# Optimization experiments

Measured on AMD Instinct MI355X. Metric: run time of the kernel, lower is better.

## Reference

```python
import jax, jax.numpy as jnp
import numpy as np

B, S, H = 2, 2048, 2048
NH, NKV = 16, 4
HD = H // NH            # 128
GROUPS = NH // NKV      # 4
ROTARY_BASE = 10000.0
NEG = -1e9


def setup_inputs() -> dict:
    key = jax.random.key(0)
    ks = jax.random.split(key, 6)
    x = jax.random.normal(ks[0], (B, S, H), dtype=jnp.float32)
    # additive causal mask [B,1,S,S]
    causal = jnp.where(jnp.tril(jnp.ones((S, S), dtype=bool)), 0.0, NEG).astype(jnp.float32)
    attention_mask = jnp.broadcast_to(causal[None, None], (B, 1, S, S))
    position_ids = jnp.broadcast_to(jnp.arange(S, dtype=jnp.int32)[None], (B, S))
    sc = 0.02
    Wq = jax.random.normal(ks[1], (H, NH * HD), dtype=jnp.float32) * sc
    Wk = jax.random.normal(ks[2], (H, NKV * HD), dtype=jnp.float32) * sc
    Wv = jax.random.normal(ks[3], (H, NKV * HD), dtype=jnp.float32) * sc
    Wo = jax.random.normal(ks[4], (H, H), dtype=jnp.float32) * sc
    return {"x": x, "attention_mask": attention_mask, "position_ids": position_ids,
            "Wq": Wq, "Wk": Wk, "Wv": Wv, "Wo": Wo}


def _rotate_half(t):
    t1, t2 = t[..., : HD // 2], t[..., HD // 2:]
    return jnp.concatenate((-t2, t1), axis=-1)


def _rope_sin_cos(position_ids, dtype):
    inv_freq = 1.0 / (ROTARY_BASE ** (jnp.arange(0, HD, 2, dtype=jnp.float32) / HD))  # [HD/2]
    freqs = position_ids.astype(jnp.float32)[..., None] * inv_freq[None, None, :]      # [B,S,HD/2]
    emb = jnp.concatenate((freqs, freqs), axis=-1)                                     # [B,S,HD]
    return jnp.sin(emb).astype(dtype), jnp.cos(emb).astype(dtype)


def reference(x, attention_mask, position_ids, Wq, Wk, Wv, Wo):
    # QKV projections (no bias)
    q = (x @ Wq).reshape(B, S, NH, HD).transpose(0, 2, 1, 3)     # [B,NH,S,HD]
    k = (x @ Wk).reshape(B, S, NKV, HD).transpose(0, 2, 1, 3)    # [B,NKV,S,HD]
    v = (x @ Wv).reshape(B, S, NKV, HD).transpose(0, 2, 1, 3)
    sin, cos = _rope_sin_cos(position_ids, x.dtype)
    sin, cos = sin[:, None], cos[:, None]                         # unsqueeze head dim
    q = q * cos + _rotate_half(q) * sin
    k = k * cos + _rotate_half(k) * sin
    # GQA: repeat kv heads
    k = jnp.repeat(k, GROUPS, axis=1)                             # [B,NH,S,HD]
    v = jnp.repeat(v, GROUPS, axis=1)
    scores = jnp.einsum('bhqd,bhkd->bhqk', q, k) / jnp.sqrt(jnp.asarray(HD, x.dtype))
    scores = scores + attention_mask                              # additive causal mask
    attn = jax.nn.softmax(scores.astype(jnp.float32), axis=-1).astype(x.dtype)
    # dropout p=0.0 -> no-op
    out = jnp.einsum('bhqk,bhkd->bhqd', attn, v)                  # [B,NH,S,HD]
    out = out.transpose(0, 2, 1, 3).reshape(B, S, H)
    return out @ Wo
```

## Files before the change

### kernel.cpp

```cpp
#include <hip/hip_runtime.h>
#include <hip/hip_bf16.h>
#include <stdint.h>
#include <math.h>

#define B_ 2
#define S_ 2048
#define H_ 2048
#define NH_ 16
#define NKV_ 4
#define HD_ 128

typedef __bf16 bf16;
typedef __bf16 bf16x8 __attribute__((ext_vector_type(8)));
typedef __bf16 bf16x4 __attribute__((ext_vector_type(4)));
typedef float f32x4 __attribute__((ext_vector_type(4)));

__device__ __forceinline__ void async_copy16(const void* g, void* l) {
  __builtin_amdgcn_global_load_lds(
      (const __attribute__((address_space(1))) void*)(uintptr_t)g,
      (__attribute__((address_space(3))) void*)(uintptr_t)l,
      16, 0, 0);
}

__device__ __forceinline__ f32x4 mfma16(bf16x8 a, bf16x8 b, f32x4 c) {
  return __builtin_amdgcn_mfma_f32_16x16x32_bf16(a, b, c, 0, 0, 0);
}


__global__ void f32_to_bf16_k(const float* __restrict__ in, bf16* __restrict__ o, int n) {
  int i = (blockIdx.x * 256 + threadIdx.x) * 4;
  if (i >= n) return;
  float4 v = *(const float4*)(in + i);
  bf16x4 r;
  r[0] = (bf16)v.x; r[1] = (bf16)v.y; r[2] = (bf16)v.z; r[3] = (bf16)v.w;
  *(bf16x4*)(o + i) = r;
}

__global__ void transpose_all_k(const float* __restrict__ Wq, const float* __restrict__ Wk,
                                const float* __restrict__ Wv, const float* __restrict__ Wo,
                                bf16* __restrict__ WqkvT, bf16* __restrict__ WoT) {
  __shared__ float tile[32][33];
  int bid = blockIdx.x;
  const float* W; bf16* Wt; int N, bx, by;
  if (bid < 4096)      { W = Wq; Wt = WqkvT;                          N = 2048; int b2 = bid;        bx = b2 & 63; by = b2 >> 6; }
  else if (bid < 5120) { W = Wk; Wt = WqkvT + (size_t)2048 * 2048;    N = 512;  int b2 = bid - 4096; bx = b2 & 15; by = b2 >> 4; }
  else if (bid < 6144) { W = Wv; Wt = WqkvT + (size_t)2560 * 2048;    N = 512;  int b2 = bid - 5120; bx = b2 & 15; by = b2 >> 4; }
  else                 { W = Wo; Wt = WoT;                            N = 2048; int b2 = bid - 6144; bx = b2 & 63; by = b2 >> 6; }
  const int K = 2048;
  int n0 = bx * 32, k0 = by * 32;
  int tx = threadIdx.x, ty = threadIdx.y;
#pragma unroll
  for (int j = 0; j < 32; j += 8)
    tile[ty + j][tx] = W[(size_t)(k0 + ty + j) * N + n0 + tx];
  __syncthreads();
#pragma unroll
  for (int j = 0; j < 32; j += 8)
    Wt[(size_t)(n0 + ty + j) * K + k0 + tx] = (bf16)tile[tx][ty + j];
}

__global__ void rope_table_k(float2* __restrict__ tab) {
  int i = blockIdx.x * 256 + threadIdx.x;
  int p = i >> 6, d = i & 63;
  float invf = expf(-((float)(2 * d) / 128.0f) * 9.210340371976184f);
  float fr = (float)p * invf;
  float sv, cv;
  sincosf(fr, &sv, &cv);
  tab[i] = make_float2(cv, sv);
}

__global__ void rope_apply_v8_k(bf16* __restrict__ t, const int* __restrict__ pos_ids,
                                const float2* __restrict__ tab, int hshift, int hmask,
                                float scale) {
  int i = blockIdx.x * 256 + threadIdx.x;
  int g = i & 7;
  int tmp = i >> 3;
  int h = tmp & hmask;
  int row = tmp >> hshift;
  int pos = pos_ids[row];
  size_t base = (((size_t)row << hshift) + h) * HD_ + g * 8;
  const float2* tb = tab + pos * 64 + g * 8;
  bf16x8 lo = *(const bf16x8*)(t + base);
  bf16x8 hi = *(const bf16x8*)(t + base + 64);
  float4 t0 = *(const float4*)(tb);
  float4 t1 = *(const float4*)(tb + 2);
  float4 t2 = *(const float4*)(tb + 4);
  float4 t3 = *(const float4*)(tb + 6);
  float cs[8], sn[8];
  cs[0]=t0.x; sn[0]=t0.y; cs[1]=t0.z; sn[1]=t0.w;
  cs[2]=t1.x; sn[2]=t1.y; cs[3]=t1.z; sn[3]=t1.w;
  cs[4]=t2.x; sn[4]=t2.y; cs[5]=t2.z; sn[5]=t2.w;
  cs[6]=t3.x; sn[6]=t3.y; cs[7]=t3.z; sn[7]=t3.w;
  bf16x8 olo, ohi;
#pragma unroll
  for (int j = 0; j < 8; ++j) {
    float a = (float)lo[j], b = (float)hi[j];
    olo[j] = (bf16)((a * cs[j] - b * sn[j]) * scale);
    ohi[j] = (bf16)((b * cs[j] + a * sn[j]) * scale);
  }
  *(bf16x8*)(t + base) = olo;
  *(bf16x8*)(t + base + 64) = ohi;
}


template <int MODE, int NJ>
__global__ __launch_bounds__(512) void gemm256_k(const bf16* __restrict__ A,
                                                 const bf16* __restrict__ Bt,
                                                 void* __restrict__ C0,
                                                 void* __restrict__ C1,
                                                 void* __restrict__ C2,
                                                 int M, int N, int K) {
  extern __shared__ __align__(16) char smem[];
  constexpr int BUFSZ = 32768 + NJ * 8192;
  const int tid = threadIdx.x;
  const int lane = tid & 63;
  const int w = tid >> 6;
  const int wm = w >> 2;
  const int wn = w & 3;
  const int g16 = lane >> 4, c16 = lane & 15;
  const int row0 = blockIdx.y * 256;
  const int col0 = blockIdx.x * (NJ * 64);
  const int srow = tid >> 3;
  const int sslot = tid & 7;
  const int ldsw = w * 1024;

  auto stage = [&](int buf, int kt, int r) {
    int rr = (r < 4) ? r : r - 4;
    int row = rr * 64 + srow;
    int ss = sslot ^ (row & 7);
    const bf16* src = (r < 4) ? (A + (size_t)(row0 + row) * K)
                              : (Bt + (size_t)(col0 + row) * K);
    async_copy16(src + (kt << 6) + ss * 8,
                 smem + buf * BUFSZ + ((r < 4) ? 0 : 32768) + rr * 8192 + ldsw);
  };

  int offA[2][8], offB[2][NJ];
#pragma unroll
  for (int ks = 0; ks < 2; ++ks) {
#pragma unroll
    for (int i = 0; i < 8; ++i) {
      int ra = wm * 128 + i * 16 + c16;
      offA[ks][i] = ra * 128 + (((ks * 4 + g16) ^ (ra & 7)) << 4);
    }
#pragma unroll
    for (int j = 0; j < NJ; ++j) {
      int rb = wn * (16 * NJ) + j * 16 + c16;
      offB[ks][j] = 32768 + rb * 128 + (((ks * 4 + g16) ^ (rb & 7)) << 4);
    }
  }

  const f32x4 fz = {0.f, 0.f, 0.f, 0.f};
  f32x4 acc[8][NJ];
#pragma unroll
  for (int i = 0; i < 8; ++i)
#pragma unroll
    for (int j = 0; j < NJ; ++j) acc[i][j] = fz;

  const int nkt = K >> 6;
#pragma unroll
  for (int r = 0; r < 4 + NJ; ++r) stage(0, 0, r);
  asm volatile("s_waitcnt vmcnt(0)" ::: "memory");
  __builtin_amdgcn_s_barrier();

  for (int t = 0; t < nkt; ++t) {
    const char* Ab = smem + (t & 1) * BUFSZ;
    const bool pf = (t + 1 < nkt);
    const int nb = (t + 1) & 1;
    bf16x8 bfr[2][NJ];

    {
      bf16x8 af[2][2];
#pragma unroll
      for (int ks = 0; ks < 2; ++ks) {
#pragma unroll
        for (int j = 0; j < NJ; ++j) bfr[ks][j] = *(const bf16x8*)(Ab + offB[ks][j]);
        af[ks][0] = *(const bf16x8*)(Ab + offA[ks][0]);
        af[ks][1] = *(const bf16x8*)(Ab + offA[ks][1]);
      }
      if (pf) { stage(nb, t + 1, 0); stage(nb, t + 1, 1); stage(nb, t + 1, 2); stage(nb, t + 1, 3); }
      __builtin_amdgcn_s_barrier();
      asm volatile("s_waitcnt lgkmcnt(0)" ::: "memory");
      __builtin_amdgcn_sched_barrier(0);
      __builtin_amdgcn_s_setprio(1);
#pragma unroll
      for (int ks = 0; ks < 2; ++ks)
#pragma unroll
        for (int m = 0; m < 2; ++m)
#pragma unroll
          for (int j = 0; j < NJ; ++j)
            acc[m][j] = mfma16(af[ks][m], bfr[ks][j], acc[m][j]);
      __builtin_amdgcn_s_setprio(0);
      __builtin_amdgcn_sched_barrier(0);
      __builtin_amdgcn_s_barrier();
    }

#pragma unroll
    for (int q = 1; q < 4; ++q) {
      bf16x8 af[2][2];
#pragma unroll
      for (int ks = 0; ks < 2; ++ks) {
        af[ks][0] = *(const bf16x8*)(Ab + offA[ks][q * 2]);
        af[ks][1] = *(const bf16x8*)(Ab + offA[ks][q * 2 + 1]);
      }
      if (q == 1 && pf) {
#pragma unroll
        for (int r = 0; r < NJ; ++r) stage(nb, t + 1, 4 + r);
      }
      __builtin_amdgcn_s_barrier();
      asm volatile("s_waitcnt lgkmcnt(0)" ::: "memory");
      __builtin_amdgcn_sched_barrier(0);
      __builtin_amdgcn_s_setprio(1);
#pragma unroll
      for (int ks = 0; ks < 2; ++ks)
#pragma unroll
        for (int m = 0; m < 2; ++m)
#pragma unroll
          for (int j = 0; j < NJ; ++j)
            acc[q * 2 + m][j] = mfma16(af[ks][m], bfr[ks][j], acc[q * 2 + m][j]);
      __builtin_amdgcn_s_setprio(0);
      __builtin_amdgcn_sched_barrier(0);
      if (q == 3 && pf) asm volatile("s_waitcnt vmcnt(0)" ::: "memory");
      __builtin_amdgcn_s_barrier();
    }
  }

#pragma unroll
  for (int i = 0; i < 8; ++i) {
    int gr0 = row0 + wm * 128 + i * 16 + g16 * 4;
#pragma unroll
    for (int j = 0; j < NJ; ++j) {
      int gc = col0 + wn * (16 * NJ) + j * 16 + c16;
      if constexpr (MODE == 2) {
        if (gc < 2048) {
#pragma unroll
          for (int r = 0; r < 4; ++r)
            ((bf16*)C0)[(size_t)(gr0 + r) * 2048 + gc] = (bf16)acc[i][j][r];
        } else if (gc < 2560) {
#pragma unroll
          for (int r = 0; r < 4; ++r)
            ((bf16*)C1)[(size_t)(gr0 + r) * 512 + (gc - 2048)] = (bf16)acc[i][j][r];
        } else {
          int dv = gc - 2560;
          int hkv = dv >> 7, d = dv & 127;
          size_t va = (((size_t)(gr0 >> 11) * NKV_ + hkv) * HD_ + d) * S_ + (gr0 & 2047);
          bf16x4 pk;
#pragma unroll
          for (int r = 0; r < 4; ++r) pk[r] = (bf16)acc[i][j][r];
          *(bf16x4*)((bf16*)C2 + va) = pk;
        }
      } else {
#pragma unroll
        for (int r = 0; r < 4; ++r) {
          if constexpr (MODE == 1)
            ((float*)C0)[(size_t)(gr0 + r) * N + gc] = acc[i][j][r];
          else
            ((bf16*)C0)[(size_t)(gr0 + r) * N + gc] = (bf16)acc[i][j][r];
        }
      }
    }
  }
}


template <int MODE>
__global__ __launch_bounds__(512) void gemm8_k(const bf16* __restrict__ A,
                                               const bf16* __restrict__ Bt,
                                               void* __restrict__ C0,
                                               void* __restrict__ C1,
                                               void* __restrict__ C2,
                                               int M, int N, int K) {
  extern __shared__ __align__(16) char smem[];
  const int tid = threadIdx.x;
  const int lane = tid & 63;
  const int w = tid >> 6;
  const int wm = w >> 2;
  const int wn = w & 3;
  const int g16 = lane >> 4, c16 = lane & 15;
  const int row0 = blockIdx.y * 128;
  const int col0 = blockIdx.x * 256;
  const int srow = tid >> 3;
  const int sslot = tid & 7;
  const int ldsw = w * 1024;

  auto stageA = [&](int s, int kt, int r) {
    int row = r * 64 + srow;
    int ss = sslot ^ (row & 7);
    async_copy16(A + (size_t)(row0 + row) * K + (kt << 6) + ss * 8,
                 smem + s * 49152 + r * 8192 + ldsw);
  };
  auto stageB = [&](int s, int kt, int r) {
    int row = r * 64 + srow;
    int ss = sslot ^ (row & 7);
    async_copy16(Bt + (size_t)(col0 + row) * K + (kt << 6) + ss * 8,
                 smem + s * 49152 + 16384 + r * 8192 + ldsw);
  };

  int offA[2][4], offB[2][4];
#pragma unroll
  for (int ks = 0; ks < 2; ++ks) {
#pragma unroll
    for (int i = 0; i < 4; ++i) {
      int ra = wm * 64 + i * 16 + c16;
      offA[ks][i] = ra * 128 + (((ks * 4 + g16) ^ (ra & 7)) << 4);
      int rb = wn * 64 + i * 16 + c16;
      offB[ks][i] = rb * 128 + (((ks * 4 + g16) ^ (rb & 7)) << 4);
    }
  }

  const f32x4 fz = {0.f, 0.f, 0.f, 0.f};
  f32x4 acc[4][4];
#pragma unroll
  for (int i = 0; i < 4; ++i)
#pragma unroll
    for (int j = 0; j < 4; ++j) acc[i][j] = fz;

  const int nkt = K >> 6;
#pragma unroll
  for (int r = 0; r < 2; ++r) stageA(0, 0, r);
#pragma unroll
  for (int r = 0; r < 4; ++r) stageB(0, 0, r);
#pragma unroll
  for (int r = 0; r < 2; ++r) stageA(1, 1, r);
#pragma unroll
  for (int r = 0; r < 4; ++r) stageB(1, 1, r);
  asm volatile("s_waitcnt vmcnt(6)" ::: "memory");
  __builtin_amdgcn_s_barrier();

  int ct = 0, pt = 2;
  for (int t = 0; t < nkt; ++t) {
    const char* Ab = smem + ct * 49152;
    const char* Bb = Ab + 16384;
    const bool pf = (t + 2 < nkt);
    const int kpf = t + 2;
    bf16x8 af[4], bfr[4];

#pragma unroll
    for (int i = 0; i < 4; ++i) af[i] = *(const bf16x8*)(Ab + offA[0][i]);
#pragma unroll
    for (int j = 0; j < 4; ++j) bfr[j] = *(const bf16x8*)(Bb + offB[0][j]);
    if (pf) { stageA(pt, kpf, 0); stageA(pt, kpf, 1); stageB(pt, kpf, 0); }
    __builtin_amdgcn_s_barrier();
    asm volatile("s_waitcnt lgkmcnt(0)" ::: "memory");
    __builtin_amdgcn_sched_barrier(0);
    __builtin_amdgcn_s_setprio(1);
#pragma unroll
    for (int i = 0; i < 4; ++i)
#pragma unroll
      for (int j = 0; j < 4; ++j) acc[i][j] = mfma16(af[i], bfr[j], acc[i][j]);
    __builtin_amdgcn_s_setprio(0);
    __builtin_amdgcn_sched_barrier(0);
    __builtin_amdgcn_s_barrier();

#pragma unroll
    for (int i = 0; i < 4; ++i) af[i] = *(const bf16x8*)(Ab + offA[1][i]);
#pragma unroll
    for (int j = 0; j < 4; ++j) bfr[j] = *(const bf16x8*)(Bb + offB[1][j]);
    if (pf) { stageB(pt, kpf, 1); stageB(pt, kpf, 2); stageB(pt, kpf, 3); }
    if (pf) asm volatile("s_waitcnt vmcnt(6)" ::: "memory");
    else    asm volatile("s_waitcnt vmcnt(0)" ::: "memory");
    __builtin_amdgcn_s_barrier();
    asm volatile("s_waitcnt lgkmcnt(0)" ::: "memory");
    __builtin_amdgcn_sched_barrier(0);
    __builtin_amdgcn_s_setprio(1);
#pragma unroll
    for (int i = 0; i < 4; ++i)
#pragma unroll
      for (int j = 0; j < 4; ++j) acc[i][j] = mfma16(af[i], bfr[j], acc[i][j]);
    __builtin_amdgcn_s_setprio(0);
    __builtin_amdgcn_sched_barrier(0);
    __builtin_amdgcn_s_barrier();

    ct = (ct == 2) ? 0 : ct + 1;
    pt = (pt == 2) ? 0 : pt + 1;
  }

#pragma unroll
  for (int i = 0; i < 4; ++i) {
    int gr0 = row0 + wm * 64 + i * 16 + g16 * 4;
#pragma unroll
    for (int j = 0; j < 4; ++j) {
      int gc = col0 + wn * 64 + j * 16 + c16;
#pragma unroll
      for (int r = 0; r < 4; ++r) {
        if constexpr (MODE == 1)
          ((float*)C0)[(size_t)(gr0 + r) * N + gc] = acc[i][j][r];
        else
          ((bf16*)C0)[(size_t)(gr0 + r) * N + gc] = (bf16)acc[i][j][r];
      }
    }
  }
}


__global__ __launch_bounds__(256, 2) void attn_fwd_k(const bf16* __restrict__ Qg,
                                                     const bf16* __restrict__ Kg,
                                                     const bf16* __restrict__ VTg,
                                                     bf16* __restrict__ Og) {
  __shared__ __align__(16) bf16 Ks[2][64 * 128];
  __shared__ __align__(16) bf16 Vt[3][128 * 64];

  const int tid = threadIdx.x;
  const int lane = tid & 63;
  const int w = tid >> 6;
  const int g16 = lane >> 4;
  const int c16 = lane & 15;

  int bid = blockIdx.x;
  int rr_ = bid >> 5, bh = bid & 31;
  int qb = (rr_ < 8) ? (15 - rr_) : (rr_ - 8);
  const int b = bh >> 4;
  const int h = bh & 15;
  const int hkv = h >> 2;
  const int q0 = qb * 128;
  const int qw = q0 + w * 32;

  bf16x8 qf[2][4];
#pragma unroll
  for (int nq = 0; nq < 2; ++nq)
#pragma unroll
    for (int ksq = 0; ksq < 4; ++ksq)
      qf[nq][ksq] = *(const bf16x8*)(Qg + ((size_t)(b * S_ + qw + nq * 16 + c16) * NH_ + h) * HD_ + (ksq * 4 + g16) * 8);

  float m_run[2] = {-1e30f, -1e30f};
  float l_run[2] = {0.f, 0.f};
  const f32x4 fz = {0.f, 0.f, 0.f, 0.f};
  f32x4 acc[2][8];
#pragma unroll
  for (int nq = 0; nq < 2; ++nq)
#pragma unroll
    for (int dt = 0; dt < 8; ++dt) acc[nq][dt] = fz;

  const size_t kbase = ((size_t)b * S_ * NKV_ + hkv) * HD_;
  const size_t vbase = ((size_t)(b * NKV_ + hkv)) * HD_ * S_;

  auto stageK = [&](int buf, int kv0) {
#pragma unroll
    for (int rd = 0; rd < 4; ++rd) {
      int Lb = rd * 256 + w * 64;
      int row = (Lb + lane) >> 4;
      int ssl = (lane & 15) ^ (row & 7);
      async_copy16(Kg + kbase + (size_t)(kv0 + row) * (NKV_ * HD_) + ssl * 8,
                   (char*)&Ks[buf][0] + Lb * 16);
    }
  };
  auto stageV = [&](int buf, int kv0) {
#pragma unroll
    for (int rd = 0; rd < 4; ++rd) {
      int Lb = rd * 256 + w * 64;
      int row = (Lb + lane) >> 3;
      int ssl = (lane & 7) ^ (row & 7);
      async_copy16(VTg + vbase + (size_t)row * S_ + kv0 + ssl * 8,
                   (char*)&Vt[buf][0] + Lb * 16);
    }
  };

  const int ntiles = 2 * qb + 2;
  stageK(0, 0);
  stageV(0, 0);

  bf16x8 pa[2][2];
  bool pend = false;
  int vb_pend = 0;
  int vbt = 0;

  for (int t = 0; t < ntiles; ++t) {
    __syncthreads();
    int vbn = (vbt == 2) ? 0 : vbt + 1;
    if (t + 1 < ntiles) { stageK((t + 1) & 1, (t + 1) * 64); stageV(vbn, (t + 1) * 64); }
    const int kv0 = t * 64;
    const bool g = (kv0 <= qw + 31);

    f32x4 sc[2][4];
    if (g) {
      const char* KsC = (const char*)&Ks[t & 1][0];
#pragma unroll
      for (int nq = 0; nq < 2; ++nq)
#pragma unroll
        for (int mt = 0; mt < 4; ++mt) sc[nq][mt] = fz;

      __builtin_amdgcn_s_setprio(1);
#pragma unroll
      for (int ksq = 0; ksq < 4; ++ksq) {
        bf16x8 kf[4];
#pragma unroll
        for (int mt = 0; mt < 4; ++mt) {
          int gp = c16 >> 2, rp = c16 & 3;
          int blk = 8 * (mt >> 1) + 2 * gp + ((mt & 1) ^ (gp & 1));
          int row = blk * 4 + rp;
          kf[mt] = *(const bf16x8*)(KsC + row * 256 + (((ksq * 4 + g16) ^ (row & 7)) << 4));
        }
#pragma unroll
        for (int nq = 0; nq < 2; ++nq)
#pragma unroll
          for (int mt = 0; mt < 4; ++mt)
            sc[nq][mt] = mfma16(kf[mt], qf[nq][ksq], sc[nq][mt]);
      }
      __builtin_amdgcn_s_setprio(0);
    }

    if (pend) {
      const char* VtP = (const char*)&Vt[vb_pend][0];
      __builtin_amdgcn_s_setprio(1);
#pragma unroll
      for (int ks = 0; ks < 2; ++ks)
#pragma unroll
        for (int dt = 0; dt < 8; ++dt) {
          int rv = dt * 16 + c16;
          bf16x8 vf = *(const bf16x8*)(VtP + rv * 128 + (((ks * 4 + g16) ^ (rv & 7)) << 4));
          acc[0][dt] = mfma16(vf, pa[0][ks], acc[0][dt]);
          acc[1][dt] = mfma16(vf, pa[1][ks], acc[1][dt]);
        }
      __builtin_amdgcn_s_setprio(0);
      pend = false;
    }

    if (g) {
      if (kv0 + 63 > qw) {
#pragma unroll
        for (int nq = 0; nq < 2; ++nq) {
          int qa = qw + nq * 16 + c16;
#pragma unroll
          for (int mt = 0; mt < 4; ++mt) {
            int blk = 8 * (mt >> 1) + 2 * g16 + ((mt & 1) ^ (g16 & 1));
#pragma unroll
            for (int r = 0; r < 4; ++r) {
              int ka = kv0 + blk * 4 + r;
              if (ka > qa) sc[nq][mt][r] = -1e30f;
            }
          }
        }
      }

      float mx[2];
#pragma unroll
      for (int nq = 0; nq < 2; ++nq) {
        float v = sc[nq][0][0];
#pragma unroll
        for (int mt = 0; mt < 4; ++mt)
#pragma unroll
          for (int r = 0; r < 4; ++r) v = fmaxf(v, sc[nq][mt][r]);
        v = fmaxf(v, __shfl_xor(v, 16));
        v = fmaxf(v, __shfl_xor(v, 32));
        mx[nq] = v;
      }
      if (__any((mx[0] > m_run[0] + 8.f) || (mx[1] > m_run[1] + 8.f))) {
#pragma unroll
        for (int nq = 0; nq < 2; ++nq) {
          float mn = fmaxf(m_run[nq], mx[nq]);
          float corr = exp2f(m_run[nq] - mn);
          m_run[nq] = mn;
          l_run[nq] *= corr;
#pragma unroll
          for (int dt = 0; dt < 8; ++dt) acc[nq][dt] *= corr;
        }
      }
#pragma unroll
      for (int nq = 0; nq < 2; ++nq) {
        float sum = 0.f;
#pragma unroll
        for (int mt = 0; mt < 4; ++mt)
#pragma unroll
          for (int r = 0; r < 4; ++r) {
            float p = exp2f(sc[nq][mt][r] - m_run[nq]);
            sc[nq][mt][r] = p;
            sum += p;
          }
        sum += __shfl_xor(sum, 16);
        sum += __shfl_xor(sum, 32);
        l_run[nq] += sum;
      }

#pragma unroll
      for (int nq = 0; nq < 2; ++nq)
#pragma unroll
        for (int ks = 0; ks < 2; ++ks) {
          f32x4 sA = (g16 & 1) ? sc[nq][2 * ks + 1] : sc[nq][2 * ks];
          f32x4 sB = (g16 & 1) ? sc[nq][2 * ks] : sc[nq][2 * ks + 1];
          bf16x8 tf;
          tf[0] = (bf16)sA[0]; tf[1] = (bf16)sA[1]; tf[2] = (bf16)sA[2]; tf[3] = (bf16)sA[3];
          tf[4] = (bf16)sB[0]; tf[5] = (bf16)sB[1]; tf[6] = (bf16)sB[2]; tf[7] = (bf16)sB[3];
          pa[nq][ks] = tf;
        }
      pend = true;
      vb_pend = vbt;
    }
    vbt = vbn;
  }

  if (pend) {
    const char* VtP = (const char*)&Vt[vb_pend][0];
#pragma unroll
    for (int ks = 0; ks < 2; ++ks)
#pragma unroll
      for (int dt = 0; dt < 8; ++dt) {
        int rv = dt * 16 + c16;
        bf16x8 vf = *(const bf16x8*)(VtP + rv * 128 + (((ks * 4 + g16) ^ (rv & 7)) << 4));
        acc[0][dt] = mfma16(vf, pa[0][ks], acc[0][dt]);
        acc[1][dt] = mfma16(vf, pa[1][ks], acc[1][dt]);
      }
  }

#pragma unroll
  for (int nq = 0; nq < 2; ++nq) {
    float inv = 1.0f / l_run[nq];
    size_t base = ((size_t)(b * S_ + qw + nq * 16 + c16) * NH_ + h) * HD_ + g16 * 4;
#pragma unroll
    for (int dt = 0; dt < 8; ++dt) {
      bf16x4 ov;
#pragma unroll
      for (int r = 0; r < 4; ++r) ov[r] = (bf16)(acc[nq][dt][r] * inv);
      *(bf16x4*)(Og + base + dt * 16) = ov;
    }
  }
}


extern "C" void kernel_launch(void* const* d_in, const int* in_sizes, int n_in,
                              void* d_out, int out_size, void* d_ws, size_t ws_size,
                              hipStream_t stream) {
  const float* x  = (const float*)d_in[0];
  const int* pos  = (const int*)d_in[2];
  const float* Wq = (const float*)d_in[3];
  const float* Wk = (const float*)d_in[4];
  const float* Wv = (const float*)d_in[5];
  const float* Wo = (const float*)d_in[6];

  char* ws = (char*)d_ws;
  size_t off = 0;
  auto alloc = [&](size_t bytes) -> char* {
    char* p = ws + off;
    off += (bytes + 255) & ~(size_t)255;
    return p;
  };
  const size_t rows = (size_t)B_ * S_;
  bf16* xb    = (bf16*)alloc(rows * H_ * 2);
  bf16* bq    = (bf16*)alloc(rows * (NH_ * HD_) * 2);
  bf16* batt  = (bf16*)alloc(rows * (NH_ * HD_) * 2);
  bf16* WqkvT = (bf16*)alloc((size_t)3072 * H_ * 2);
  bf16* WoT   = (bf16*)alloc((size_t)H_ * H_ * 2);
  bf16* bk    = (bf16*)alloc(rows * (NKV_ * HD_) * 2);
  bf16* VT    = (bf16*)alloc(rows * (NKV_ * HD_) * 2);
  float2* tab = (float2*)alloc((size_t)S_ * 64 * sizeof(float2));

  auto* fqkv = gemm256_k<2, 3>;
  auto* fo   = gemm8_k<1>;
  const int lds256 = 2 * (32768 + 3 * 8192);
  const int lds8   = 3 * 49152;
  bool big =
      (hipFuncSetAttribute((const void*)fqkv, hipFuncAttributeMaxDynamicSharedMemorySize, lds256) == hipSuccess) &&
      (hipFuncSetAttribute((const void*)fo, hipFuncAttributeMaxDynamicSharedMemorySize, lds8) == hipSuccess);

  f32_to_bf16_k<<<(rows * H_) / (256 * 4), 256, 0, stream>>>(x, xb, rows * H_);
  transpose_all_k<<<10240, dim3(32, 8), 0, stream>>>(Wq, Wk, Wv, Wo, WqkvT, WoT);
  rope_table_k<<<(S_ * 64) / 256, 256, 0, stream>>>(tab);

  gemm256_k<2, 3><<<dim3(16, 16), 512, lds256, stream>>>(xb, WqkvT, bq, bk, VT, 4096, 3072, 2048);
  (void)big;

  rope_apply_v8_k<<<(4096 * NH_ * 8) / 256, 256, 0, stream>>>(bq, pos, tab, 4, 15, 0.12753102f);
  rope_apply_v8_k<<<(4096 * NKV_ * 8) / 256, 256, 0, stream>>>(bk, pos, tab, 2, 3, 1.0f);

  attn_fwd_k<<<dim3(512), 256, 0, stream>>>(bq, bk, VT, batt);

  gemm8_k<1><<<dim3(8, 32), 512, lds8, stream>>>(batt, WoT, d_out, nullptr, nullptr, 4096, 2048, 2048);
}
```

Baseline: 199.2 us.

## Merge prep kernels, simplify attention pipeline, reorder causal block scheduling

Merges the fp32-to-bf16 cast, weight transposes and RoPE table build into one launch to cut launch overhead. Replaces the attention kernel's deferred PV software pipeline (triple-buffered V) with a simpler double buffer where PV runs right after softmax in the same iteration. Also remaps block indices so heavy and light causal q-blocks are interleaved across the grid. The PV step no longer overlaps the next tile's QK and softmax work, which may expose latency, but the kernel uses less LDS and fewer registers.

```diff
diff --git a/kernel.cpp b/kernel.cpp
--- a/kernel.cpp
+++ b/kernel.cpp
@@ -27,45 +27,46 @@
 }
 
 
-__global__ void f32_to_bf16_k(const float* __restrict__ in, bf16* __restrict__ o, int n) {
-  int i = (blockIdx.x * 256 + threadIdx.x) * 4;
-  if (i >= n) return;
-  float4 v = *(const float4*)(in + i);
-  bf16x4 r;
-  r[0] = (bf16)v.x; r[1] = (bf16)v.y; r[2] = (bf16)v.z; r[3] = (bf16)v.w;
-  *(bf16x4*)(o + i) = r;
-}
-
-__global__ void transpose_all_k(const float* __restrict__ Wq, const float* __restrict__ Wk,
-                                const float* __restrict__ Wv, const float* __restrict__ Wo,
-                                bf16* __restrict__ WqkvT, bf16* __restrict__ WoT) {
+__global__ void prep_all_k(const float* __restrict__ x,
+                           const float* __restrict__ Wq, const float* __restrict__ Wk,
+                           const float* __restrict__ Wv, const float* __restrict__ Wo,
+                           bf16* __restrict__ xb, bf16* __restrict__ WqkvT,
+                           bf16* __restrict__ WoT, float2* __restrict__ tab) {
   __shared__ float tile[32][33];
-  int bid = blockIdx.x;
-  const float* W; bf16* Wt; int N, bx, by;
-  if (bid < 4096)      { W = Wq; Wt = WqkvT;                          N = 2048; int b2 = bid;        bx = b2 & 63; by = b2 >> 6; }
-  else if (bid < 5120) { W = Wk; Wt = WqkvT + (size_t)2048 * 2048;    N = 512;  int b2 = bid - 4096; bx = b2 & 15; by = b2 >> 4; }
-  else if (bid < 6144) { W = Wv; Wt = WqkvT + (size_t)2560 * 2048;    N = 512;  int b2 = bid - 5120; bx = b2 & 15; by = b2 >> 4; }
-  else                 { W = Wo; Wt = WoT;                            N = 2048; int b2 = bid - 6144; bx = b2 & 63; by = b2 >> 6; }
-  const int K = 2048;
-  int n0 = bx * 32, k0 = by * 32;
-  int tx = threadIdx.x, ty = threadIdx.y;
-#pragma unroll
-  for (int j = 0; j < 32; j += 8)
-    tile[ty + j][tx] = W[(size_t)(k0 + ty + j) * N + n0 + tx];
-  __syncthreads();
-#pragma unroll
-  for (int j = 0; j < 32; j += 8)
-    Wt[(size_t)(n0 + ty + j) * K + k0 + tx] = (bf16)tile[tx][ty + j];
-}
-
-__global__ void rope_table_k(float2* __restrict__ tab) {
-  int i = blockIdx.x * 256 + threadIdx.x;
-  int p = i >> 6, d = i & 63;
-  float invf = expf(-((float)(2 * d) / 128.0f) * 9.210340371976184f);
-  float fr = (float)p * invf;
-  float sv, cv;
-  sincosf(fr, &sv, &cv);
-  tab[i] = make_float2(cv, sv);
+  const int bid = blockIdx.x;
+  const int tid = threadIdx.x;
+
+  if (bid < 10240) {
+    const float* W; bf16* Wt; int N, bx, by;
+    if (bid < 4096)      { W = Wq; Wt = WqkvT;                       N = 2048; int b2 = bid;        bx = b2 & 63; by = b2 >> 6; }
+    else if (bid < 5120) { W = Wk; Wt = WqkvT + (size_t)2048 * 2048; N = 512;  int b2 = bid - 4096; bx = b2 & 15; by = b2 >> 4; }
+    else if (bid < 6144) { W = Wv; Wt = WqkvT + (size_t)2560 * 2048; N = 512;  int b2 = bid - 5120; bx = b2 & 15; by = b2 >> 4; }
+    else                 { W = Wo; Wt = WoT;                         N = 2048; int b2 = bid - 6144; bx = b2 & 63; by = b2 >> 6; }
+    const int K = 2048;
+    int n0 = bx * 32, k0 = by * 32;
+    int tx = tid & 31, ty = tid >> 5;
+#pragma unroll
+    for (int j = 0; j < 32; j += 8)
+      tile[ty + j][tx] = W[(size_t)(k0 + ty + j) * N + n0 + tx];
+    __syncthreads();
+#pragma unroll
+    for (int j = 0; j < 32; j += 8)
+      Wt[(size_t)(n0 + ty + j) * K + k0 + tx] = (bf16)tile[tx][ty + j];
+  } else if (bid < 18432) {
+    int i = ((bid - 10240) * 256 + tid) * 4;
+    float4 v = *(const float4*)(x + i);
+    bf16x4 r;
+    r[0] = (bf16)v.x; r[1] = (bf16)v.y; r[2] = (bf16)v.z; r[3] = (bf16)v.w;
+    *(bf16x4*)(xb + i) = r;
+  } else {
+    int i = (bid - 18432) * 256 + tid;
+    int p = i >> 6, d = i & 63;
+    float invf = expf(-((float)(2 * d) / 128.0f) * 9.210340371976184f);
+    float fr = (float)p * invf;
+    float sv, cv;
+    sincosf(fr, &sv, &cv);
+    tab[i] = make_float2(cv, sv);
+  }
 }
 
 __global__ void rope_apply_v8_k(bf16* __restrict__ t, const int* __restrict__ pos_ids,
@@ -396,7 +397,7 @@
                                                      const bf16* __restrict__ VTg,
                                                      bf16* __restrict__ Og) {
   __shared__ __align__(16) bf16 Ks[2][64 * 128];
-  __shared__ __align__(16) bf16 Vt[3][128 * 64];
+  __shared__ __align__(16) bf16 Vt[2][128 * 64];
 
   const int tid = threadIdx.x;
   const int lane = tid & 63;
@@ -404,9 +405,11 @@
   const int g16 = lane >> 4;
   const int c16 = lane & 15;
 
-  int bid = blockIdx.x;
-  int rr_ = bid >> 5, bh = bid & 31;
-  int qb = (rr_ < 8) ? (15 - rr_) : (rr_ - 8);
+  const int bid = blockIdx.x;
+  const int i_ = ((bid >> 8) << 7) | ((bid & 255) >> 1);
+  const int par = ((bid & 1) ^ (bid >> 8)) & 1;
+  const int qb = par ? (i_ >> 5) : (15 - (i_ >> 5));
+  const int bh = i_ & 31;
   const int b = bh >> 4;
   const int h = bh & 15;
   const int hkv = h >> 2;
@@ -432,7 +435,7 @@
   const size_t kbase = ((size_t)b * S_ * NKV_ + hkv) * HD_;
   const size_t vbase = ((size_t)(b * NKV_ + hkv)) * HD_ * S_;
 
-  auto stageK = [&](int buf, int kv0) {
+  auto stage = [&](int buf, int kv0) {
 #pragma unroll
     for (int rd = 0; rd < 4; ++rd) {
       int Lb = rd * 256 + w * 64;
@@ -441,8 +444,6 @@
       async_copy16(Kg + kbase + (size_t)(kv0 + row) * (NKV_ * HD_) + ssl * 8,
                    (char*)&Ks[buf][0] + Lb * 16);
     }
-  };
-  auto stageV = [&](int buf, int kv0) {
 #pragma unroll
     for (int rd = 0; rd < 4; ++rd) {
       int Lb = rd * 256 + w * 64;
@@ -454,24 +455,19 @@
   };
 
   const int ntiles = 2 * qb + 2;
-  stageK(0, 0);
-  stageV(0, 0);
-
-  bf16x8 pa[2][2];
-  bool pend = false;
-  int vb_pend = 0;
-  int vbt = 0;
+  stage(0, 0);
+  int cur = 0;
 
   for (int t = 0; t < ntiles; ++t) {
     __syncthreads();
-    int vbn = (vbt == 2) ? 0 : vbt + 1;
-    if (t + 1 < ntiles) { stageK((t + 1) & 1, (t + 1) * 64); stageV(vbn, (t + 1) * 64); }
+    if (t + 1 < ntiles) stage(cur ^ 1, (t + 1) * 64);
     const int kv0 = t * 64;
-    const bool g = (kv0 <= qw + 31);
-
-    f32x4 sc[2][4];
-    if (g) {
-      const char* KsC = (const char*)&Ks[t & 1][0];
+
+    if (kv0 <= qw + 31) {
+      const bf16* KsC = &Ks[cur][0];
+      const bf16* VtC = &Vt[cur][0];
+
+      f32x4 sc[2][4];
 #pragma unroll
       for (int nq = 0; nq < 2; ++nq)
 #pragma unroll
@@ -486,7 +482,7 @@
           int gp = c16 >> 2, rp = c16 & 3;
           int blk = 8 * (mt >> 1) + 2 * gp + ((mt & 1) ^ (gp & 1));
           int row = blk * 4 + rp;
-          kf[mt] = *(const bf16x8*)(KsC + row * 256 + (((ksq * 4 + g16) ^ (row & 7)) << 4));
+          kf[mt] = *(const bf16x8*)((const char*)KsC + row * 256 + (((ksq * 4 + g16) ^ (row & 7)) << 4));
         }
 #pragma unroll
         for (int nq = 0; nq < 2; ++nq)
@@ -495,25 +491,7 @@
             sc[nq][mt] = mfma16(kf[mt], qf[nq][ksq], sc[nq][mt]);
       }
       __builtin_amdgcn_s_setprio(0);
-    }
-
-    if (pend) {
-      const char* VtP = (const char*)&Vt[vb_pend][0];
-      __builtin_amdgcn_s_setprio(1);
-#pragma unroll
-      for (int ks = 0; ks < 2; ++ks)
-#pragma unroll
-        for (int dt = 0; dt < 8; ++dt) {
-          int rv = dt * 16 + c16;
-          bf16x8 vf = *(const bf16x8*)(VtP + rv * 128 + (((ks * 4 + g16) ^ (rv & 7)) << 4));
-          acc[0][dt] = mfma16(vf, pa[0][ks], acc[0][dt]);
-          acc[1][dt] = mfma16(vf, pa[1][ks], acc[1][dt]);
-        }
-      __builtin_amdgcn_s_setprio(0);
-      pend = false;
-    }
-
-    if (g) {
+
       if (kv0 + 63 > qw) {
 #pragma unroll
         for (int nq = 0; nq < 2; ++nq) {
@@ -569,6 +547,7 @@
         l_run[nq] += sum;
       }
 
+      bf16x8 pa[2][2];
 #pragma unroll
       for (int nq = 0; nq < 2; ++nq)
 #pragma unroll
@@ -580,23 +559,20 @@
           tf[4] = (bf16)sB[0]; tf[5] = (bf16)sB[1]; tf[6] = (bf16)sB[2]; tf[7] = (bf16)sB[3];
           pa[nq][ks] = tf;
         }
-      pend = true;
-      vb_pend = vbt;
-    }
-    vbt = vbn;
-  }
-
-  if (pend) {
-    const char* VtP = (const char*)&Vt[vb_pend][0];
-#pragma unroll
-    for (int ks = 0; ks < 2; ++ks)
-#pragma unroll
-      for (int dt = 0; dt < 8; ++dt) {
-        int rv = dt * 16 + c16;
-        bf16x8 vf = *(const bf16x8*)(VtP + rv * 128 + (((ks * 4 + g16) ^ (rv & 7)) << 4));
-        acc[0][dt] = mfma16(vf, pa[0][ks], acc[0][dt]);
-        acc[1][dt] = mfma16(vf, pa[1][ks], acc[1][dt]);
-      }
+
+      __builtin_amdgcn_s_setprio(1);
+#pragma unroll
+      for (int ks = 0; ks < 2; ++ks)
+#pragma unroll
+        for (int dt = 0; dt < 8; ++dt) {
+          int rv = dt * 16 + c16;
+          bf16x8 vf = *(const bf16x8*)((const char*)VtC + rv * 128 + (((ks * 4 + g16) ^ (rv & 7)) << 4));
+          acc[0][dt] = mfma16(vf, pa[0][ks], acc[0][dt]);
+          acc[1][dt] = mfma16(vf, pa[1][ks], acc[1][dt]);
+        }
+      __builtin_amdgcn_s_setprio(0);
+    }
+    cur ^= 1;
   }
 
 #pragma unroll
@@ -645,16 +621,12 @@
   auto* fo   = gemm8_k<1>;
   const int lds256 = 2 * (32768 + 3 * 8192);
   const int lds8   = 3 * 49152;
-  bool big =
-      (hipFuncSetAttribute((const void*)fqkv, hipFuncAttributeMaxDynamicSharedMemorySize, lds256) == hipSuccess) &&
-      (hipFuncSetAttribute((const void*)fo, hipFuncAttributeMaxDynamicSharedMemorySize, lds8) == hipSuccess);
-
-  f32_to_bf16_k<<<(rows * H_) / (256 * 4), 256, 0, stream>>>(x, xb, rows * H_);
-  transpose_all_k<<<10240, dim3(32, 8), 0, stream>>>(Wq, Wk, Wv, Wo, WqkvT, WoT);
-  rope_table_k<<<(S_ * 64) / 256, 256, 0, stream>>>(tab);
+  (void)hipFuncSetAttribute((const void*)fqkv, hipFuncAttributeMaxDynamicSharedMemorySize, lds256);
+  (void)hipFuncSetAttribute((const void*)fo, hipFuncAttributeMaxDynamicSharedMemorySize, lds8);
+
+  prep_all_k<<<18944, 256, 0, stream>>>(x, Wq, Wk, Wv, Wo, xb, WqkvT, WoT, tab);
 
   gemm256_k<2, 3><<<dim3(16, 16), 512, lds256, stream>>>(xb, WqkvT, bq, bk, VT, 4096, 3072, 2048);
-  (void)big;
 
   rope_apply_v8_k<<<(4096 * NH_ * 8) / 256, 256, 0, stream>>>(bq, pos, tab, 4, 15, 0.12753102f);
   rope_apply_v8_k<<<(4096 * NKV_ * 8) / 256, 256, 0, stream>>>(bk, pos, tab, 2, 3, 1.0f);
```

Result: faster. 193.8 us, median of 2 (-2.7%).
